# Kernel optimization log

Measured on AMD Instinct MI355X. Metric: run time of the kernel, lower is better.

The kernel has to match this reference:

```python
import jax, jax.numpy as jnp
import numpy as np

B, TENC, LIS = 32, 2048, 512
HID, EMB, CLS = 512, 256, 64
KEY, VAL, TDEC = 128, 128, 65


def setup_inputs() -> dict:
    key = jax.random.key(0)
    ks = jax.random.split(key, 32)
    s = 0.02
    p = lambda i, shape: jax.random.normal(ks[i], shape, jnp.float32) * s
    return {
        "listener_output": jax.random.normal(ks[0], (B, TENC, LIS), jnp.float32),
        "outputs_length": jax.random.randint(ks[1], (B,), TENC // 2, TENC + 1, jnp.int32),
        "padded_targets": jax.random.randint(ks[2], (B, TDEC), 0, CLS, jnp.int32),
        "teacher_forcing": 1,
        "embed_table": p(3, (CLS, EMB)),
        "W_ih1": p(4, (4 * HID, EMB + VAL)), "W_hh1": p(5, (4 * HID, HID)),
        "b_ih1": p(6, (4 * HID,)), "b_hh1": p(7, (4 * HID,)),
        "W_ih2": p(8, (4 * HID, HID)), "W_hh2": p(9, (4 * HID, HID)),
        "b_ih2": p(10, (4 * HID,)), "b_hh2": p(11, (4 * HID,)),
        "W_s": p(12, (KEY, HID)), "b_s": p(13, (KEY,)),
        "W_h": p(14, (KEY, LIS)), "b_h": p(15, (KEY,)),
        "W_v": p(16, (VAL, LIS)), "b_v": p(17, (VAL,)),
        "W_c": p(18, (CLS, HID + VAL)), "b_c": p(19, (CLS,)),
        "h1_0": p(20, (B, HID)), "c1_0": p(21, (B, HID)),
        "h2_0": p(22, (B, HID)), "c2_0": p(23, (B, HID)),
    }


def _lstm_cell(x, h, c, Wih, Whh, bih, bhh):
    # torch LSTMCell gate order: input, forget, cell, output
    g = x @ Wih.T + bih + h @ Whh.T + bhh
    i, f, gg, o = jnp.split(g, 4, axis=-1)
    c = jax.nn.sigmoid(f) * c + jax.nn.sigmoid(i) * jnp.tanh(gg)
    h = jax.nn.sigmoid(o) * jnp.tanh(c)
    return h, c


def _speller(listener_output, outputs_length, padded_targets, teacher_forcing,
             embed_table, W_ih1, W_hh1, b_ih1, b_hh1, W_ih2, W_hh2, b_ih2, b_hh2,
             W_s, b_s, W_h, b_h, W_v, b_v, W_c, b_c, h1_0, c1_0, h2_0, c2_0):
    Bv, Tenc, _ = listener_output.shape
    timestep = padded_targets.shape[1] - 1
    # time-validity mask; row 0 is left unmasked, matching the original loops (i != 0)
    valid = jnp.arange(Tenc)[None, :] < outputs_length[:, None]          # [B, Tenc]
    row0 = (jnp.arange(Bv) == 0)[:, None]
    mask = jnp.where(row0, True, valid).astype(listener_output.dtype)    # [B, Tenc]
    # key/value projections are step-invariant: hoist out of the loop (same math)
    key_enc = listener_output @ W_h.T + b_h                              # [B, Tenc, KEY]
    value = (listener_output @ W_v.T + b_v) * mask[:, :, None]           # [B, Tenc, VAL]
    tf = jnp.asarray(teacher_forcing, jnp.float32)
    tf_key = jax.random.key(1)
    samp_key = jax.random.key(2)

    def step(carry, i):
        h1, c1, h2, c2, context, preds = carry
        # teacher-forcing coin (np.random.random() < teacher_forcing)
        coin = jax.random.uniform(jax.random.fold_in(tf_key, i)) < tf
        tok = jnp.where(coin, padded_targets[:, jnp.maximum(i - 1, 0)], preds)
        x = jnp.concatenate([embed_table[tok], context], axis=1)
        nh1, nc1 = _lstm_cell(x, h1, c1, W_ih1, W_hh1, b_ih1, b_hh1)
        nh2, nc2 = _lstm_cell(nh1, h2, c2, W_ih2, W_hh2, b_ih2, b_hh2)
        first = i == 0   # step 0 uses the learned initial states, no RNN update
        h1 = jnp.where(first, h1, nh1); c1 = jnp.where(first, c1, nc1)
        h2 = jnp.where(first, h2, nh2); c2 = jnp.where(first, c2, nc2)
        query = h2 @ W_s.T + b_s                                         # [B, KEY]
        energy = jnp.einsum('bk,btk->bt', query, key_enc)                # [B, Tenc]
        att = jax.nn.softmax(energy, axis=1) * mask
        att = att / jnp.maximum(att.sum(axis=1, keepdims=True), 1e-12)   # F.normalize p=1
        context = jnp.einsum('bt,btv->bv', att, value)                   # [B, VAL]
        logits = jnp.concatenate([h2, context], axis=1) @ W_c.T + b_c    # [B, CLS]
        preds = jax.random.categorical(jax.random.fold_in(samp_key, i), logits).astype(jnp.int32)
        return (h1, c1, h2, c2, context, preds), (logits, preds, att)

    init = (h1_0, c1_0, h2_0, c2_0,
            jnp.zeros((Bv, W_v.shape[0]), listener_output.dtype),
            jnp.zeros((Bv,), jnp.int32))
    _, (logits, preds, atts) = jax.lax.scan(step, init, jnp.arange(timestep))
    # logits: [T, B, CLS] (the per-step probs list), preds -> [B, T], atts: [T, B, Tenc]
    return logits, preds.T, atts


def reference(listener_output, outputs_length, padded_targets, teacher_forcing,
              embed_table, W_ih1, W_hh1, b_ih1, b_hh1, W_ih2, W_hh2, b_ih2, b_hh2,
              W_s, b_s, W_h, b_h, W_v, b_v, W_c, b_c, h1_0, c1_0, h2_0, c2_0):
    return _speller(listener_output, outputs_length, padded_targets, teacher_forcing,
                    embed_table, W_ih1, W_hh1, b_ih1, b_hh1, W_ih2, W_hh2, b_ih2, b_hh2,
                    W_s, b_s, W_h, b_h, W_v, b_v, W_c, b_c, h1_0, c1_0, h2_0, c2_0)
```

## Files before the change

### kernel.cpp

```cpp
#include <hip/hip_runtime.h>
#include <stdint.h>
#include <stddef.h>


struct BarCtr { unsigned v; unsigned pad[31]; };

struct P {
  const float* listener; const int* outlen; const int* ptgt;
  const float* embed;
  const float *W_ih1, *W_hh1, *b_ih1, *b_hh1;
  const float *W_ih2, *W_hh2, *b_ih2, *b_hh2;
  const float *W_s, *b_s, *W_h, *b_h, *W_v, *b_v, *W_c, *b_c;
  const float *h1_0, *c1_0, *h2_0, *c2_0;
  float* keyT;
  float* value;
  float* h1;
  float* c1;
  float* h2;
  float* c2;
  float* wbuf;
  float* ctxnum;
  float* Ssum;
  BarCtr* bar;
  float* out;
};

__device__ __forceinline__ float sigf(float x) { return 1.0f / (1.0f + expf(-x)); }

__device__ __forceinline__ float gload(const float* p) {
  return __hip_atomic_load(p, __ATOMIC_RELAXED, __HIP_MEMORY_SCOPE_AGENT);
}
__device__ __forceinline__ void gstore(float* p, float v) {
  __hip_atomic_store(p, v, __ATOMIC_RELAXED, __HIP_MEMORY_SCOPE_AGENT);
}
__device__ __forceinline__ void gadd(float* p, float v) {
  __hip_atomic_fetch_add(p, v, __ATOMIC_RELAXED, __HIP_MEMORY_SCOPE_AGENT);
}

__device__ __forceinline__ void tf2x32(uint32_t k0, uint32_t k1,
                                       uint32_t x0, uint32_t x1,
                                       uint32_t& o0, uint32_t& o1) {
  uint32_t k2 = k0 ^ k1 ^ 0x1BD11BDAu;
#define TFR(r) { x0 += x1; x1 = (x1 << (r)) | (x1 >> (32 - (r))); x1 ^= x0; }
  x0 += k0; x1 += k1;
  TFR(13) TFR(15) TFR(26) TFR(6)   x0 += k1; x1 += k2 + 1u;
  TFR(17) TFR(29) TFR(16) TFR(24)  x0 += k2; x1 += k0 + 2u;
  TFR(13) TFR(15) TFR(26) TFR(6)   x0 += k0; x1 += k1 + 3u;
  TFR(17) TFR(29) TFR(16) TFR(24)  x0 += k1; x1 += k2 + 4u;
  TFR(13) TFR(15) TFR(26) TFR(6)   x0 += k2; x1 += k0 + 5u;
#undef TFR
  o0 = x0; o1 = x1;
}

__device__ __forceinline__ float gumbel_f(uint32_t bits) {
  float f = __uint_as_float((bits >> 9) | 0x3f800000u) - 1.0f;
  float u = (f == 0.0f) ? 1.17549435e-38f : f;
  return -logf(-logf(u));
}

__device__ __forceinline__ void gbar(BarCtr* bar, int blk, unsigned round) {
  __syncthreads();
  if (threadIdx.x == 0) {
    __hip_atomic_fetch_add(&bar[blk & 7].v, 1u, __ATOMIC_RELAXED, __HIP_MEMORY_SCOPE_AGENT);
    const unsigned tgt = round * 256u;
    for (;;) {
      unsigned s = 0;
#pragma unroll
      for (int c = 0; c < 8; ++c)
        s += __hip_atomic_load(&bar[c].v, __ATOMIC_RELAXED, __HIP_MEMORY_SCOPE_AGENT);
      if (s >= tgt) break;
      __builtin_amdgcn_s_sleep(1);
    }
    asm volatile("" ::: "memory");
  }
  __syncthreads();
}

__global__ void __launch_bounds__(256) k_init(P p) {
  int idx = blockIdx.x * 256 + threadIdx.x;
  p.h1[idx] = p.h1_0[idx];
  p.c1[idx] = p.c1_0[idx];
  p.h2[idx] = p.h2_0[idx];
  p.c2[idx] = p.c2_0[idx];
  if (idx < 8192) p.ctxnum[idx] = 0.0f;
  if (idx < 64)   p.Ssum[idx]   = 0.0f;
  if (idx < 8)    p.bar[idx].v  = 0u;
}

__global__ void __launch_bounds__(256) k_proj(P p) {
  const int blk = blockIdx.x, tid = threadIdx.x;
  const int b = blk >> 7, tb = blk & 127, t0 = tb * 16;
  __shared__ float lst[16 * 512];
  const float* src = p.listener + ((size_t)b * 2048 + t0) * 512;
  for (int n = 0; n < 32; ++n) {
    int idx = n * 256 + tid;
    lst[idx] = src[idx];
  }
  __syncthreads();
  const int c = tid;
  const float* wr = (c < 128) ? (p.W_h + c * 512) : (p.W_v + (c - 128) * 512);
  const float bias = (c < 128) ? p.b_h[c] : p.b_v[c - 128];
  float acc[16];
#pragma unroll
  for (int r = 0; r < 16; ++r) acc[r] = 0.0f;
  for (int k4 = 0; k4 < 128; ++k4) {
    float4 w4 = ((const float4*)wr)[k4];
#pragma unroll
    for (int r = 0; r < 16; ++r) {
      float4 x4 = ((const float4*)(lst + r * 512))[k4];
      acc[r] = fmaf(w4.x, x4.x, fmaf(w4.y, x4.y, fmaf(w4.z, x4.z, fmaf(w4.w, x4.w, acc[r]))));
    }
  }
  if (c < 128) {
#pragma unroll
    for (int r = 0; r < 16; ++r)
      p.keyT[((size_t)b * 128 + c) * 2048 + t0 + r] = acc[r] + bias;
  } else {
#pragma unroll
    for (int r = 0; r < 16; ++r)
      p.value[((size_t)b * 2048 + t0 + r) * 128 + (c - 128)] = acc[r] + bias;
  }
}

__device__ void do_finalize(const P& p, int step, int b, int tid, float* sf) {
  const int c = tid;
  const int par = step & 1;
  const float* h2p  = p.h2 + par * 16384 + b * 512;
  const float* ctxp = p.ctxnum + par * 4096 + b * 128;
  const float invS = 1.0f / fmaxf(gload(&p.Ssum[par * 32 + b]), 1e-12f);
#pragma unroll
  for (int n = 0; n < 10; ++n) {
    int idx = n * 64 + c;
    float v = (idx < 512) ? gload(&h2p[idx]) : gload(&ctxp[idx - 512]) * invS;
    sf[idx] = v;
  }
  asm volatile("s_waitcnt vmcnt(0) lgkmcnt(0)" ::: "memory");
  __builtin_amdgcn_wave_barrier();
  const float* wr = p.W_c + c * 640;
  float a0 = 0.f, a1 = 0.f, a2 = 0.f, a3 = 0.f;
#pragma unroll 8
  for (int k4 = 0; k4 < 160; ++k4) {
    float4 w4 = ((const float4*)wr)[k4];
    float4 x4 = ((const float4*)sf)[k4];
    a0 = fmaf(w4.x, x4.x, a0); a1 = fmaf(w4.y, x4.y, a1);
    a2 = fmaf(w4.z, x4.z, a2); a3 = fmaf(w4.w, x4.w, a3);
  }
  float lg = p.b_c[c] + ((a0 + a1) + (a2 + a3));
  p.out[(size_t)(step * 32 + b) * 64 + c] = lg;
  uint32_t n0, n1, r0, r1;
  tf2x32(0u, 2u, 0u, (uint32_t)step, n0, n1);
  tf2x32(n0, n1, 0u, (uint32_t)(b * 64 + c), r0, r1);
  float z = gumbel_f(r0 ^ r1) + lg;
  int ix = c;
  for (int off = 32; off; off >>= 1) {
    float zz = __shfl_xor(z, off, 64); int ii = __shfl_xor(ix, off, 64);
    if (zz > z || (zz == z && ii < ix)) { z = zz; ix = ii; }
  }
  if (c == 0) p.out[131072 + b * 64 + step] = (float)ix;
}

__device__ void phase_g1(const P& p, int i, float* smem, int* smi, int blk, int tid) {
  const int par = i & 1, q1 = par ^ 1;
  float* sx   = smem;
  float* sp   = smem + 4224;
  float* sg   = smem + 5248;
  float* sinv = smem + 5504;
  if (tid < 256) {
    int flat = blk * 256 + tid;
    int b = flat >> 11, t = flat & 2047;
    float s = fmaxf(gload(&p.Ssum[q1 * 32 + b]), 1e-12f);
    p.out[133120 + (size_t)((i - 1) * 32 + b) * 2048 + t] = gload(&p.wbuf[b * 2048 + t]) / s;
  }
  if (tid < 32) {
    sinv[tid] = 1.0f / fmaxf(gload(&p.Ssum[q1 * 32 + tid]), 1e-12f);
    smi[tid]  = p.ptgt[tid * 65 + (i - 1)];
  }
  const int b = tid & 31, m = (tid >> 5) & 7, q = tid >> 8;
  const int j0 = blk * 2;
  const int row = j0 + (m & 1) + (m >> 1) * 512;
  const float* h1r  = p.h1 + q1 * 16384;
  const float* ctxr = p.ctxnum + q1 * 4096;
  float a0 = 0.f, a1 = 0.f, a2 = 0.f, a3 = 0.f;
  for (int kt = 0; kt < 7; ++kt) {
    __syncthreads();
#pragma unroll
    for (int n = 0; n < 4; ++n) {
      int idx = n * 1024 + tid, fb = idx >> 7, kk = idx & 127;
      float v;
      if (kt < 2)       v = p.embed[smi[fb] * 256 + kt * 128 + kk];
      else if (kt == 2) v = gload(&ctxr[fb * 128 + kk]) * sinv[fb];
      else              v = gload(&h1r[fb * 512 + (kt - 3) * 128 + kk]);
      sx[fb * 132 + kk] = v;
    }
    __syncthreads();
    const float* wr = (kt < 3) ? (p.W_ih1 + row * 384 + kt * 128)
                               : (p.W_hh1 + row * 512 + (kt - 3) * 128);
    const float4* w4p = (const float4*)(wr + q * 32);
    const float4* x4p = (const float4*)(sx + b * 132 + q * 32);
#pragma unroll
    for (int k4 = 0; k4 < 8; ++k4) {
      float4 w4 = w4p[k4], x4 = x4p[k4];
      a0 = fmaf(w4.x, x4.x, a0); a1 = fmaf(w4.y, x4.y, a1);
      a2 = fmaf(w4.z, x4.z, a2); a3 = fmaf(w4.w, x4.w, a3);
    }
  }
  sp[q * 256 + m * 32 + b] = (a0 + a1) + (a2 + a3);
  __syncthreads();
  if (tid < 256) {
    int mm = tid >> 5;
    int rr = j0 + (mm & 1) + (mm >> 1) * 512;
    sg[tid] = sp[tid] + sp[256 + tid] + sp[512 + tid] + sp[768 + tid]
            + p.b_ih1[rr] + p.b_hh1[rr];
  }
  __syncthreads();
  if (tid < 64) {
    int jl = tid >> 5, bb = tid & 31, j = j0 + jl;
    float gi = sg[(0 + jl) * 32 + bb];
    float gf = sg[(2 + jl) * 32 + bb];
    float gg = sg[(4 + jl) * 32 + bb];
    float go = sg[(6 + jl) * 32 + bb];
    float cp = p.c1[q1 * 16384 + bb * 512 + j];
    float c  = sigf(gf) * cp + sigf(gi) * tanhf(gg);
    gstore(&p.h1[par * 16384 + bb * 512 + j], sigf(go) * tanhf(c));
    p.c1[par * 16384 + bb * 512 + j] = c;
  }
  if (blk < 32 && tid < 64) do_finalize(p, i - 1, blk, tid, smem);
}

__device__ void phase_g2(const P& p, int i, float* smem, int blk, int tid) {
  const int par = i & 1, q1 = par ^ 1;
  float* sx = smem;
  float* sp = smem + 4224;
  float* sg = smem + 5248;
  if (blk < 4) gstore(&p.ctxnum[q1 * 4096 + blk * 1024 + tid], 0.0f);
  if (blk == 4 && tid < 32) gstore(&p.Ssum[q1 * 32 + tid], 0.0f);
  const int b = tid & 31, m = (tid >> 5) & 7, q = tid >> 8;
  const int j0 = blk * 2;
  const int row = j0 + (m & 1) + (m >> 1) * 512;
  const float* h1r = p.h1 + par * 16384;
  const float* h2r = p.h2 + q1 * 16384;
  float a0 = 0.f, a1 = 0.f, a2 = 0.f, a3 = 0.f;
  for (int kt = 0; kt < 8; ++kt) {
    __syncthreads();
#pragma unroll
    for (int n = 0; n < 4; ++n) {
      int idx = n * 1024 + tid, fb = idx >> 7, kk = idx & 127;
      float v = (kt < 4) ? gload(&h1r[fb * 512 + kt * 128 + kk])
                         : gload(&h2r[fb * 512 + (kt - 4) * 128 + kk]);
      sx[fb * 132 + kk] = v;
    }
    __syncthreads();
    const float* wr = (kt < 4) ? (p.W_ih2 + row * 512 + kt * 128)
                               : (p.W_hh2 + row * 512 + (kt - 4) * 128);
    const float4* w4p = (const float4*)(wr + q * 32);
    const float4* x4p = (const float4*)(sx + b * 132 + q * 32);
#pragma unroll
    for (int k4 = 0; k4 < 8; ++k4) {
      float4 w4 = w4p[k4], x4 = x4p[k4];
      a0 = fmaf(w4.x, x4.x, a0); a1 = fmaf(w4.y, x4.y, a1);
      a2 = fmaf(w4.z, x4.z, a2); a3 = fmaf(w4.w, x4.w, a3);
    }
  }
  sp[q * 256 + m * 32 + b] = (a0 + a1) + (a2 + a3);
  __syncthreads();
  if (tid < 256) {
    int mm = tid >> 5;
    int rr = j0 + (mm & 1) + (mm >> 1) * 512;
    sg[tid] = sp[tid] + sp[256 + tid] + sp[512 + tid] + sp[768 + tid]
            + p.b_ih2[rr] + p.b_hh2[rr];
  }
  __syncthreads();
  if (tid < 64) {
    int jl = tid >> 5, bb = tid & 31, j = j0 + jl;
    float gi = sg[(0 + jl) * 32 + bb];
    float gf = sg[(2 + jl) * 32 + bb];
    float gg = sg[(4 + jl) * 32 + bb];
    float go = sg[(6 + jl) * 32 + bb];
    float cp = p.c2[q1 * 16384 + bb * 512 + j];
    float c  = sigf(gf) * cp + sigf(gi) * tanhf(gg);
    gstore(&p.h2[par * 16384 + bb * 512 + j], sigf(go) * tanhf(c));
    p.c2[par * 16384 + bb * 512 + j] = c;
  }
}

__device__ __forceinline__ void phase_att(const P& p, int i, float* smem, const float* kslice,
                                          const float va[32], int blk, int tid) {
  const int par = i & 1;
  const int b = blk >> 3;
  float* sh2 = smem;
  float* sq  = smem + 512;
  float* sqp = smem + 640;
  float* se  = smem + 1152;
  float* sw  = smem + 2176;
  float* swr = smem + 2432;
  float* sc  = smem + 2440;
  const float* h2p = p.h2 + par * 16384 + b * 512;
  if (tid < 512) sh2[tid] = gload(&h2p[tid]);
  __syncthreads();
  if (tid < 512) {
    int col = tid & 127, qh = tid >> 7;
    const float* wr = p.W_s + col * 512 + qh * 128;
    const float4* h4p = (const float4*)(sh2 + qh * 128);
    float a0 = 0.f, a1 = 0.f, a2 = 0.f, a3 = 0.f;
#pragma unroll
    for (int j4 = 0; j4 < 32; ++j4) {
      float4 w4 = ((const float4*)wr)[j4], h4 = h4p[j4];
      a0 = fmaf(w4.x, h4.x, a0); a1 = fmaf(w4.y, h4.y, a1);
      a2 = fmaf(w4.z, h4.z, a2); a3 = fmaf(w4.w, h4.w, a3);
    }
    sqp[qh * 128 + col] = (a0 + a1) + (a2 + a3);
  }
  __syncthreads();
  if (tid < 128) sq[tid] = p.b_s[tid] + sqp[tid] + sqp[128 + tid] + sqp[256 + tid] + sqp[384 + tid];
  __syncthreads();
  {
    int tt = tid & 255, kq = tid >> 8;
    const float* kc = kslice + tt;
    const int kb = kq * 32;
    float e0 = 0.f, e1 = 0.f, e2 = 0.f, e3 = 0.f;
#pragma unroll 8
    for (int k = 0; k < 32; k += 4) {
      e0 = fmaf(kc[(kb + k + 0) * 256], sq[kb + k + 0], e0);
      e1 = fmaf(kc[(kb + k + 1) * 256], sq[kb + k + 1], e1);
      e2 = fmaf(kc[(kb + k + 2) * 256], sq[kb + k + 2], e2);
      e3 = fmaf(kc[(kb + k + 3) * 256], sq[kb + k + 3], e3);
    }
    se[kq * 256 + tt] = (e0 + e1) + (e2 + e3);
  }
  __syncthreads();
  if (tid < 256) {
    const int ch = blk & 7, t0 = ch * 256;
    int t = t0 + tid;
    float e = se[tid] + se[256 + tid] + se[512 + tid] + se[768 + tid];
    const int len = p.outlen[b];
    bool msk = (b == 0) || (t < len);
    float wv = msk ? expf(e) : 0.0f;
    gstore(&p.wbuf[b * 2048 + t], wv);
    sw[tid] = wv;
    float s = wv;
    for (int off = 32; off; off >>= 1) s += __shfl_xor(s, off, 64);
    if ((tid & 63) == 0) swr[tid >> 6] = s;
  }
  __syncthreads();
  if (tid == 0) gadd(&p.Ssum[par * 32 + b], swr[0] + swr[1] + swr[2] + swr[3]);
  {
    int v = tid & 127, tp = tid >> 7;
    float c0 = 0.f, c1v = 0.f;
#pragma unroll
    for (int tt2 = 0; tt2 < 32; tt2 += 2) {
      c0  = fmaf(sw[tp * 32 + tt2],     va[tt2],     c0);
      c1v = fmaf(sw[tp * 32 + tt2 + 1], va[tt2 + 1], c1v);
    }
    sc[tp * 128 + v] = c0 + c1v;
  }
  __syncthreads();
  if (tid < 128) {
    float s = 0.f;
#pragma unroll
    for (int tp = 0; tp < 8; ++tp) s += sc[tp * 128 + tid];
    gadd(&p.ctxnum[par * 4096 + b * 128 + tid], s);
  }
}

__global__ void __launch_bounds__(1024, 4) k_loop(P p) {
  __shared__ __align__(16) float kslice[128 * 256];
  __shared__ __align__(16) float smem[5600];
  __shared__ int smi[32];
  const int blk = blockIdx.x, tid = threadIdx.x;
  const int b_att = blk >> 3, ch = blk & 7, t0 = ch * 256;
  {
    const float* ksrc = p.keyT + (size_t)b_att * 262144 + t0;
    for (int n = 0; n < 32; ++n) {
      int idx = n * 1024 + tid;
      int k = idx >> 8, tt = idx & 255;
      kslice[k * 256 + tt] = ksrc[(size_t)k * 2048 + tt];
    }
  }
  float va[32];
  {
    int v = tid & 127, tp = tid >> 7;
    const float* vb = p.value + ((size_t)(b_att * 2048 + t0 + tp * 32)) * 128 + v;
#pragma unroll
    for (int tt2 = 0; tt2 < 32; ++tt2) va[tt2] = vb[(size_t)tt2 * 128];
  }
  __syncthreads();
  unsigned nb = 0;
  phase_att(p, 0, smem, kslice, va, blk, tid);
  for (int i = 1; i < 64; ++i) {
    gbar(p.bar, blk, ++nb);
    phase_g1(p, i, smem, smi, blk, tid);
    gbar(p.bar, blk, ++nb);
    phase_g2(p, i, smem, blk, tid);
    gbar(p.bar, blk, ++nb);
    phase_att(p, i, smem, kslice, va, blk, tid);
  }
  gbar(p.bar, blk, ++nb);
  if (tid < 256) {
    int flat = blk * 256 + tid;
    int b = flat >> 11, t = flat & 2047;
    float s = fmaxf(gload(&p.Ssum[1 * 32 + b]), 1e-12f);
    p.out[133120 + (size_t)(63 * 32 + b) * 2048 + t] = gload(&p.wbuf[b * 2048 + t]) / s;
  }
  if (blk < 32 && tid < 64) do_finalize(p, 63, blk, tid, smem);
}

extern "C" void kernel_launch(void* const* d_in, const int* in_sizes, int n_in,
                              void* d_out, int out_size, void* d_ws, size_t ws_size,
                              hipStream_t stream) {
  P p;
  p.listener = (const float*)d_in[0];
  p.outlen   = (const int*)d_in[1];
  p.ptgt     = (const int*)d_in[2];
  p.embed = (const float*)d_in[4];
  p.W_ih1 = (const float*)d_in[5];  p.W_hh1 = (const float*)d_in[6];
  p.b_ih1 = (const float*)d_in[7];  p.b_hh1 = (const float*)d_in[8];
  p.W_ih2 = (const float*)d_in[9];  p.W_hh2 = (const float*)d_in[10];
  p.b_ih2 = (const float*)d_in[11]; p.b_hh2 = (const float*)d_in[12];
  p.W_s = (const float*)d_in[13]; p.b_s = (const float*)d_in[14];
  p.W_h = (const float*)d_in[15]; p.b_h = (const float*)d_in[16];
  p.W_v = (const float*)d_in[17]; p.b_v = (const float*)d_in[18];
  p.W_c = (const float*)d_in[19]; p.b_c = (const float*)d_in[20];
  p.h1_0 = (const float*)d_in[21]; p.c1_0 = (const float*)d_in[22];
  p.h2_0 = (const float*)d_in[23]; p.c2_0 = (const float*)d_in[24];

  char* w = (char*)d_ws;
  p.keyT   = (float*)w; w += (size_t)32 * 128 * 2048 * 4;
  p.value  = (float*)w; w += (size_t)32 * 2048 * 128 * 4;
  p.h1  = (float*)w; w += 2 * 32 * 512 * 4;
  p.c1  = (float*)w; w += 2 * 32 * 512 * 4;
  p.h2  = (float*)w; w += 2 * 32 * 512 * 4;
  p.c2  = (float*)w; w += 2 * 32 * 512 * 4;
  p.wbuf   = (float*)w; w += 32 * 2048 * 4;
  p.ctxnum = (float*)w; w += 2 * 32 * 128 * 4;
  p.Ssum   = (float*)w; w += 2 * 32 * 4;
  p.bar    = (BarCtr*)w; w += 8 * sizeof(BarCtr);
  p.out = (float*)d_out;

  k_init<<<64, 256, 0, stream>>>(p);
  k_proj<<<4096, 256, 0, stream>>>(p);
  k_loop<<<256, 1024, 0, stream>>>(p);
}
```

Before: 6.090 ms.

## Transpose LSTM weights once and repartition gate GEMVs by batch and row groups

A new pre-kernel transposes and concatenates the LSTM input and hidden weight matrices into a K-major layout, with the four gates of each 16-row group placed next to each other. Each block of the persistent loop now owns 4 batch rows and 16 hidden units. It stages the inputs transposed in shared memory, and each wave reduces a K-slice with coalesced scalar weight loads, combining partial sums through shared-memory atomics. This drops the seven or eight tiled shared-memory staging rounds and their __syncthreads per LSTM phase. The cost is an extra transpose kernel, added workspace, and each block now re-reading a whole weight column strip from L2.

```diff
diff --git a/kernel.cpp b/kernel.cpp
--- a/kernel.cpp
+++ b/kernel.cpp
@@ -14,6 +14,8 @@
   const float *h1_0, *c1_0, *h2_0, *c2_0;
   float* keyT;
   float* value;
+  float* WT1;
+  float* WT2;
   float* h1;
   float* c1;
   float* h2;
@@ -122,6 +124,34 @@
   }
 }
 
+__global__ void __launch_bounds__(256) k_tw(P p) {
+  __shared__ float t[64 * 65];
+  const int blk = blockIdx.x, tid = threadIdx.x;
+  const float *Wa, *Wb; float* dst; int kt, ct, ka, sA, sB;
+  if (blk < 512) { kt = blk >> 5; ct = blk & 31; Wa = p.W_ih2; sA = 512; Wb = p.W_hh2; sB = 512; ka = 512; dst = p.WT2; }
+  else { int b2 = blk - 512; kt = b2 >> 5; ct = b2 & 31; Wa = p.W_ih1; sA = 384; Wb = p.W_hh1; sB = 512; ka = 384; dst = p.WT1; }
+  for (int n = 0; n < 4; ++n) {
+    int fid = n * 256 + tid;
+    int cl = fid >> 4, k4 = (fid & 15) * 4;
+    int grow = ((cl >> 4) * 512) + ct * 16 + (cl & 15);
+    int k = kt * 64 + k4;
+    float4 v = (k < ka) ? *(const float4*)&Wa[(size_t)grow * sA + k]
+                        : *(const float4*)&Wb[(size_t)grow * sB + (k - ka)];
+    t[cl * 65 + k4 + 0] = v.x; t[cl * 65 + k4 + 1] = v.y;
+    t[cl * 65 + k4 + 2] = v.z; t[cl * 65 + k4 + 3] = v.w;
+  }
+  __syncthreads();
+  for (int n = 0; n < 4; ++n) {
+    int fid = n * 256 + tid;
+    int kl = fid >> 4, c4 = (fid & 15) * 4;
+    int k = kt * 64 + kl;
+    float4 o;
+    o.x = t[(c4 + 0) * 65 + kl]; o.y = t[(c4 + 1) * 65 + kl];
+    o.z = t[(c4 + 2) * 65 + kl]; o.w = t[(c4 + 3) * 65 + kl];
+    *(float4*)&dst[(size_t)k * 2048 + ct * 64 + c4] = o;
+  }
+}
+
 __device__ void do_finalize(const P& p, int step, int b, int tid, float* sf) {
   const int c = tid;
   const int par = step & 1;
@@ -159,127 +189,121 @@
   if (c == 0) p.out[131072 + b * 64 + step] = (float)ix;
 }
 
-__device__ void phase_g1(const P& p, int i, float* smem, int* smi, int blk, int tid) {
+__device__ void phase_g1(const P& p, int i, float* xT, float* sg, float* sfin, int blk, int tid) {
   const int par = i & 1, q1 = par ^ 1;
-  float* sx   = smem;
-  float* sp   = smem + 4224;
-  float* sg   = smem + 5248;
-  float* sinv = smem + 5504;
+  const int bg = blk >> 5, rg = blk & 31;
   if (tid < 256) {
     int flat = blk * 256 + tid;
     int b = flat >> 11, t = flat & 2047;
     float s = fmaxf(gload(&p.Ssum[q1 * 32 + b]), 1e-12f);
     p.out[133120 + (size_t)((i - 1) * 32 + b) * 2048 + t] = gload(&p.wbuf[b * 2048 + t]) / s;
   }
-  if (tid < 32) {
-    sinv[tid] = 1.0f / fmaxf(gload(&p.Ssum[q1 * 32 + tid]), 1e-12f);
-    smi[tid]  = p.ptgt[tid * 65 + (i - 1)];
-  }
-  const int b = tid & 31, m = (tid >> 5) & 7, q = tid >> 8;
-  const int j0 = blk * 2;
-  const int row = j0 + (m & 1) + (m >> 1) * 512;
-  const float* h1r  = p.h1 + q1 * 16384;
-  const float* ctxr = p.ctxnum + q1 * 4096;
-  float a0 = 0.f, a1 = 0.f, a2 = 0.f, a3 = 0.f;
-  for (int kt = 0; kt < 7; ++kt) {
-    __syncthreads();
-#pragma unroll
-    for (int n = 0; n < 4; ++n) {
-      int idx = n * 1024 + tid, fb = idx >> 7, kk = idx & 127;
-      float v;
-      if (kt < 2)       v = p.embed[smi[fb] * 256 + kt * 128 + kk];
-      else if (kt == 2) v = gload(&ctxr[fb * 128 + kk]) * sinv[fb];
-      else              v = gload(&h1r[fb * 512 + (kt - 3) * 128 + kk]);
-      sx[fb * 132 + kk] = v;
-    }
-    __syncthreads();
-    const float* wr = (kt < 3) ? (p.W_ih1 + row * 384 + kt * 128)
-                               : (p.W_hh1 + row * 512 + (kt - 3) * 128);
-    const float4* w4p = (const float4*)(wr + q * 32);
-    const float4* x4p = (const float4*)(sx + b * 132 + q * 32);
-#pragma unroll
-    for (int k4 = 0; k4 < 8; ++k4) {
-      float4 w4 = w4p[k4], x4 = x4p[k4];
-      a0 = fmaf(w4.x, x4.x, a0); a1 = fmaf(w4.y, x4.y, a1);
-      a2 = fmaf(w4.z, x4.z, a2); a3 = fmaf(w4.w, x4.w, a3);
-    }
-  }
-  sp[q * 256 + m * 32 + b] = (a0 + a1) + (a2 + a3);
-  __syncthreads();
+  {
+    int b4 = tid & 3, kb = (tid >> 2) << 2;
+    if (kb < 896) {
+      int b = bg * 4 + b4;
+      float v0, v1, v2, v3;
+      if (kb < 256) {
+        int tok = p.ptgt[b * 65 + (i - 1)];
+        const float* e = p.embed + tok * 256 + kb;
+        v0 = e[0]; v1 = e[1]; v2 = e[2]; v3 = e[3];
+      } else if (kb < 384) {
+        float invS = 1.0f / fmaxf(gload(&p.Ssum[q1 * 32 + b]), 1e-12f);
+        const float* cx = p.ctxnum + q1 * 4096 + b * 128 + (kb - 256);
+        v0 = gload(cx + 0) * invS; v1 = gload(cx + 1) * invS;
+        v2 = gload(cx + 2) * invS; v3 = gload(cx + 3) * invS;
+      } else {
+        const float* h = p.h1 + q1 * 16384 + b * 512 + (kb - 384);
+        v0 = gload(h + 0); v1 = gload(h + 1); v2 = gload(h + 2); v3 = gload(h + 3);
+      }
+      xT[(kb + 0) * 4 + b4] = v0; xT[(kb + 1) * 4 + b4] = v1;
+      xT[(kb + 2) * 4 + b4] = v2; xT[(kb + 3) * 4 + b4] = v3;
+    }
+  }
   if (tid < 256) {
-    int mm = tid >> 5;
-    int rr = j0 + (mm & 1) + (mm >> 1) * 512;
-    sg[tid] = sp[tid] + sp[256 + tid] + sp[512 + tid] + sp[768 + tid]
-            + p.b_ih1[rr] + p.b_hh1[rr];
+    int lr = tid & 63;
+    int grow = (lr >> 4) * 512 + rg * 16 + (lr & 15);
+    sg[tid] = p.b_ih1[grow] + p.b_hh1[grow];
+  }
+  __syncthreads();
+  {
+    int w = tid >> 6, lane = tid & 63;
+    const float* wp = p.WT1 + (size_t)(w * 56) * 2048 + rg * 64 + lane;
+    const float4* xp = (const float4*)(xT + (w * 56) * 4);
+    float a0 = 0.f, a1 = 0.f, a2 = 0.f, a3 = 0.f;
+#pragma unroll 8
+    for (int k = 0; k < 56; ++k) {
+      float wv = wp[(size_t)k * 2048];
+      float4 x4 = xp[k];
+      a0 = fmaf(wv, x4.x, a0); a1 = fmaf(wv, x4.y, a1);
+      a2 = fmaf(wv, x4.z, a2); a3 = fmaf(wv, x4.w, a3);
+    }
+    atomicAdd(&sg[lane], a0);        atomicAdd(&sg[64 + lane], a1);
+    atomicAdd(&sg[128 + lane], a2);  atomicAdd(&sg[192 + lane], a3);
   }
   __syncthreads();
   if (tid < 64) {
-    int jl = tid >> 5, bb = tid & 31, j = j0 + jl;
-    float gi = sg[(0 + jl) * 32 + bb];
-    float gf = sg[(2 + jl) * 32 + bb];
-    float gg = sg[(4 + jl) * 32 + bb];
-    float go = sg[(6 + jl) * 32 + bb];
-    float cp = p.c1[q1 * 16384 + bb * 512 + j];
+    int bb = tid >> 4, jl = tid & 15;
+    int b = bg * 4 + bb, j = rg * 16 + jl;
+    float gi = sg[bb * 64 + jl];
+    float gf = sg[bb * 64 + 16 + jl];
+    float gg = sg[bb * 64 + 32 + jl];
+    float go = sg[bb * 64 + 48 + jl];
+    float cp = p.c1[q1 * 16384 + b * 512 + j];
     float c  = sigf(gf) * cp + sigf(gi) * tanhf(gg);
-    gstore(&p.h1[par * 16384 + bb * 512 + j], sigf(go) * tanhf(c));
-    p.c1[par * 16384 + bb * 512 + j] = c;
-  }
-  if (blk < 32 && tid < 64) do_finalize(p, i - 1, blk, tid, smem);
-}
-
-__device__ void phase_g2(const P& p, int i, float* smem, int blk, int tid) {
+    gstore(&p.h1[par * 16384 + b * 512 + j], sigf(go) * tanhf(c));
+    p.c1[par * 16384 + b * 512 + j] = c;
+  }
+  if (blk < 32 && tid < 64) do_finalize(p, i - 1, blk, tid, sfin);
+}
+
+__device__ void phase_g2(const P& p, int i, float* xT, float* sg, int blk, int tid) {
   const int par = i & 1, q1 = par ^ 1;
-  float* sx = smem;
-  float* sp = smem + 4224;
-  float* sg = smem + 5248;
+  const int bg = blk >> 5, rg = blk & 31;
   if (blk < 4) gstore(&p.ctxnum[q1 * 4096 + blk * 1024 + tid], 0.0f);
   if (blk == 4 && tid < 32) gstore(&p.Ssum[q1 * 32 + tid], 0.0f);
-  const int b = tid & 31, m = (tid >> 5) & 7, q = tid >> 8;
-  const int j0 = blk * 2;
-  const int row = j0 + (m & 1) + (m >> 1) * 512;
-  const float* h1r = p.h1 + par * 16384;
-  const float* h2r = p.h2 + q1 * 16384;
-  float a0 = 0.f, a1 = 0.f, a2 = 0.f, a3 = 0.f;
-  for (int kt = 0; kt < 8; ++kt) {
-    __syncthreads();
-#pragma unroll
-    for (int n = 0; n < 4; ++n) {
-      int idx = n * 1024 + tid, fb = idx >> 7, kk = idx & 127;
-      float v = (kt < 4) ? gload(&h1r[fb * 512 + kt * 128 + kk])
-                         : gload(&h2r[fb * 512 + (kt - 4) * 128 + kk]);
-      sx[fb * 132 + kk] = v;
-    }
-    __syncthreads();
-    const float* wr = (kt < 4) ? (p.W_ih2 + row * 512 + kt * 128)
-                               : (p.W_hh2 + row * 512 + (kt - 4) * 128);
-    const float4* w4p = (const float4*)(wr + q * 32);
-    const float4* x4p = (const float4*)(sx + b * 132 + q * 32);
-#pragma unroll
-    for (int k4 = 0; k4 < 8; ++k4) {
-      float4 w4 = w4p[k4], x4 = x4p[k4];
-      a0 = fmaf(w4.x, x4.x, a0); a1 = fmaf(w4.y, x4.y, a1);
-      a2 = fmaf(w4.z, x4.z, a2); a3 = fmaf(w4.w, x4.w, a3);
-    }
-  }
-  sp[q * 256 + m * 32 + b] = (a0 + a1) + (a2 + a3);
-  __syncthreads();
+  {
+    int b4 = tid & 3, kb = (tid >> 2) << 2;
+    int b = bg * 4 + b4;
+    const float* h = (kb < 512) ? (p.h1 + par * 16384 + b * 512 + kb)
+                                : (p.h2 + q1 * 16384 + b * 512 + (kb - 512));
+    float v0 = gload(h + 0), v1 = gload(h + 1), v2 = gload(h + 2), v3 = gload(h + 3);
+    xT[(kb + 0) * 4 + b4] = v0; xT[(kb + 1) * 4 + b4] = v1;
+    xT[(kb + 2) * 4 + b4] = v2; xT[(kb + 3) * 4 + b4] = v3;
+  }
   if (tid < 256) {
-    int mm = tid >> 5;
-    int rr = j0 + (mm & 1) + (mm >> 1) * 512;
-    sg[tid] = sp[tid] + sp[256 + tid] + sp[512 + tid] + sp[768 + tid]
-            + p.b_ih2[rr] + p.b_hh2[rr];
+    int lr = tid & 63;
+    int grow = (lr >> 4) * 512 + rg * 16 + (lr & 15);
+    sg[tid] = p.b_ih2[grow] + p.b_hh2[grow];
+  }
+  __syncthreads();
+  {
+    int w = tid >> 6, lane = tid & 63;
+    const float* wp = p.WT2 + (size_t)(w * 64) * 2048 + rg * 64 + lane;
+    const float4* xp = (const float4*)(xT + (w * 64) * 4);
+    float a0 = 0.f, a1 = 0.f, a2 = 0.f, a3 = 0.f;
+#pragma unroll 8
+    for (int k = 0; k < 64; ++k) {
+      float wv = wp[(size_t)k * 2048];
+      float4 x4 = xp[k];
+      a0 = fmaf(wv, x4.x, a0); a1 = fmaf(wv, x4.y, a1);
+      a2 = fmaf(wv, x4.z, a2); a3 = fmaf(wv, x4.w, a3);
+    }
+    atomicAdd(&sg[lane], a0);        atomicAdd(&sg[64 + lane], a1);
+    atomicAdd(&sg[128 + lane], a2);  atomicAdd(&sg[192 + lane], a3);
   }
   __syncthreads();
   if (tid < 64) {
-    int jl = tid >> 5, bb = tid & 31, j = j0 + jl;
-    float gi = sg[(0 + jl) * 32 + bb];
-    float gf = sg[(2 + jl) * 32 + bb];
-    float gg = sg[(4 + jl) * 32 + bb];
-    float go = sg[(6 + jl) * 32 + bb];
-    float cp = p.c2[q1 * 16384 + bb * 512 + j];
+    int bb = tid >> 4, jl = tid & 15;
+    int b = bg * 4 + bb, j = rg * 16 + jl;
+    float gi = sg[bb * 64 + jl];
+    float gf = sg[bb * 64 + 16 + jl];
+    float gg = sg[bb * 64 + 32 + jl];
+    float go = sg[bb * 64 + 48 + jl];
+    float cp = p.c2[q1 * 16384 + b * 512 + j];
     float c  = sigf(gf) * cp + sigf(gi) * tanhf(gg);
-    gstore(&p.h2[par * 16384 + bb * 512 + j], sigf(go) * tanhf(c));
-    p.c2[par * 16384 + bb * 512 + j] = c;
+    gstore(&p.h2[par * 16384 + b * 512 + j], sigf(go) * tanhf(c));
+    p.c2[par * 16384 + b * 512 + j] = c;
   }
 }
 
@@ -364,8 +388,10 @@
 
 __global__ void __launch_bounds__(1024, 4) k_loop(P p) {
   __shared__ __align__(16) float kslice[128 * 256];
-  __shared__ __align__(16) float smem[5600];
-  __shared__ int smi[32];
+  __shared__ __align__(16) float work[4096 + 256 + 640];
+  float* xT   = work;
+  float* sg   = work + 4096;
+  float* sfin = work + 4352;
   const int blk = blockIdx.x, tid = threadIdx.x;
   const int b_att = blk >> 3, ch = blk & 7, t0 = ch * 256;
   {
@@ -385,14 +411,14 @@
   }
   __syncthreads();
   unsigned nb = 0;
-  phase_att(p, 0, smem, kslice, va, blk, tid);
+  phase_att(p, 0, work, kslice, va, blk, tid);
   for (int i = 1; i < 64; ++i) {
     gbar(p.bar, blk, ++nb);
-    phase_g1(p, i, smem, smi, blk, tid);
+    phase_g1(p, i, xT, sg, sfin, blk, tid);
     gbar(p.bar, blk, ++nb);
-    phase_g2(p, i, smem, blk, tid);
+    phase_g2(p, i, xT, sg, blk, tid);
     gbar(p.bar, blk, ++nb);
-    phase_att(p, i, smem, kslice, va, blk, tid);
+    phase_att(p, i, work, kslice, va, blk, tid);
   }
   gbar(p.bar, blk, ++nb);
   if (tid < 256) {
@@ -401,7 +427,7 @@
     float s = fmaxf(gload(&p.Ssum[1 * 32 + b]), 1e-12f);
     p.out[133120 + (size_t)(63 * 32 + b) * 2048 + t] = gload(&p.wbuf[b * 2048 + t]) / s;
   }
-  if (blk < 32 && tid < 64) do_finalize(p, 63, blk, tid, smem);
+  if (blk < 32 && tid < 64) do_finalize(p, 63, blk, tid, sfin);
 }
 
 extern "C" void kernel_launch(void* const* d_in, const int* in_sizes, int n_in,
@@ -426,6 +452,8 @@
   char* w = (char*)d_ws;
   p.keyT   = (float*)w; w += (size_t)32 * 128 * 2048 * 4;
   p.value  = (float*)w; w += (size_t)32 * 2048 * 128 * 4;
+  p.WT1    = (float*)w; w += (size_t)896 * 2048 * 4;
+  p.WT2    = (float*)w; w += (size_t)1024 * 2048 * 4;
   p.h1  = (float*)w; w += 2 * 32 * 512 * 4;
   p.c1  = (float*)w; w += 2 * 32 * 512 * 4;
   p.h2  = (float*)w; w += 2 * 32 * 512 * 4;
@@ -438,5 +466,6 @@
 
   k_init<<<64, 256, 0, stream>>>(p);
   k_proj<<<4096, 256, 0, stream>>>(p);
+  k_tw<<<960, 256, 0, stream>>>(p);
   k_loop<<<256, 1024, 0, stream>>>(p);
 }
```

After: 6.134 ms. Within noise of the previous version (+0.7%).
